# Kernel tuning notes

Hardware: AMD Instinct MI355X
Metric: run time of the kernel (lower is better)

The kernel has to match this reference:

```python
import jax, jax.numpy as jnp
import numpy as np

N_NODES = 100000
N_EDGES = 1200000
D = 64            # in_channels == hidden_channels
N_GRAPHS = 512
N_CLASSES = 10
N_LAYERS = 3
BN_EPS = 1e-5


def setup_inputs() -> dict:
    key = jax.random.key(0)
    ks = jax.random.split(key, 16)
    x = jax.random.normal(ks[0], (N_NODES, D), dtype=jnp.float32)
    edge_index = jax.random.randint(ks[1], (2, N_EDGES), 0, N_NODES, dtype=jnp.int64)
    batch = jnp.sort(jax.random.randint(ks[2], (N_NODES,), 0, N_GRAPHS, dtype=jnp.int64))
    s = 1.0 / np.sqrt(D)
    # all GIN layers share shape since in_channels == hidden_channels
    mlp_w1 = jax.random.uniform(ks[3], (N_LAYERS, D, D), jnp.float32, -s, s)
    mlp_b1 = jax.random.uniform(ks[4], (N_LAYERS, D), jnp.float32, -s, s)
    mlp_w2 = jax.random.uniform(ks[5], (N_LAYERS, D, D), jnp.float32, -s, s)
    mlp_b2 = jax.random.uniform(ks[6], (N_LAYERS, D), jnp.float32, -s, s)
    bn_g = jnp.ones((N_LAYERS, D), jnp.float32)
    bn_b = jnp.zeros((N_LAYERS, D), jnp.float32)
    hw1 = jax.random.uniform(ks[7], (D, D), jnp.float32, -s, s)
    hb1 = jax.random.uniform(ks[8], (D,), jnp.float32, -s, s)
    hg1 = jnp.ones((D,), jnp.float32)
    hbb1 = jnp.zeros((D,), jnp.float32)
    hw2 = jax.random.uniform(ks[9], (D, D // 2), jnp.float32, -s, s)
    hb2 = jax.random.uniform(ks[10], (D // 2,), jnp.float32, -s, s)
    hg2 = jnp.ones((D // 2,), jnp.float32)
    hbb2 = jnp.zeros((D // 2,), jnp.float32)
    s2 = 1.0 / np.sqrt(D // 2)
    ow = jax.random.uniform(ks[11], (D // 2, N_CLASSES), jnp.float32, -s2, s2)
    ob = jax.random.uniform(ks[12], (N_CLASSES,), jnp.float32, -s2, s2)
    return dict(x=x, edge_index=edge_index, batch=batch,
                mlp_w1=mlp_w1, mlp_b1=mlp_b1, mlp_w2=mlp_w2, mlp_b2=mlp_b2,
                bn_g=bn_g, bn_b=bn_b,
                hw1=hw1, hb1=hb1, hg1=hg1, hbb1=hbb1,
                hw2=hw2, hb2=hb2, hg2=hg2, hbb2=hbb2, ow=ow, ob=ob)


def _bn(x, g, b):
    # training-mode BatchNorm1d: biased variance over the batch (node/graph) dim
    mu = jnp.mean(x, axis=0)
    var = jnp.mean((x - mu) ** 2, axis=0)
    return g * (x - mu) * jax.lax.rsqrt(var + BN_EPS) + b


def reference(x, edge_index, batch, mlp_w1, mlp_b1, mlp_w2, mlp_b2, bn_g, bn_b,
              hw1, hb1, hg1, hbb1, hw2, hb2, hg2, hbb2, ow, ob):
    src, dst = edge_index[0], edge_index[1]
    h = x
    for l in range(N_LAYERS):
        # GINConv (eps=0): h_i <- MLP(h_i + sum_{j in N(i)} h_j)
        agg = jax.ops.segment_sum(h[src], dst, num_segments=N_NODES)
        z = h + agg
        z = jax.nn.relu(z @ mlp_w1[l] + mlp_b1[l]) @ mlp_w2[l] + mlp_b2[l]
        h = jax.nn.relu(_bn(z, bn_g[l], bn_b[l]))
        # dropout omitted (deterministic eval)
    # global mean pool per graph
    sums = jax.ops.segment_sum(h, batch, num_segments=N_GRAPHS)
    cnts = jax.ops.segment_sum(jnp.ones((N_NODES,), h.dtype), batch, num_segments=N_GRAPHS)
    g = sums / jnp.maximum(cnts, 1.0)[:, None]
    g = jax.nn.relu(_bn(g @ hw1 + hb1, hg1, hbb1))
    g = jax.nn.relu(_bn(g @ hw2 + hb2, hg2, hbb2))
    return g @ ow + ob
```

## Files before the change

### kernel.cpp

```cpp
#include <hip/hip_runtime.h>
#include <hip/hip_bf16.h>

#define N_NODES 100000
#define N_EDGES 1200000
#define NG 512

typedef float f32;
typedef unsigned short u16;
typedef unsigned short us8 __attribute__((ext_vector_type(8)));
typedef __bf16 bf16x8 __attribute__((ext_vector_type(8)));
typedef float f32x16 __attribute__((ext_vector_type(16)));

__device__ __forceinline__ f32 bf2f(u16 v) {
  return __uint_as_float(((unsigned)v) << 16);
}
__device__ __forceinline__ u16 f2bf(f32 f) {
  __hip_bfloat16 b = __float2bfloat16(f);
  return *reinterpret_cast<u16*>(&b);
}

__global__ void k_detect(const int* __restrict__ w, int* __restrict__ flag) {
  int t = threadIdx.x;
  int acc = 0;
  #pragma unroll
  for (int k = 0; k < 8; ++k) acc |= w[(t * 8 + k) * 2 + 1];
  if (acc) atomicOr(flag, 1);
}

__global__ void k_count(const int* __restrict__ w, const int* __restrict__ flag,
                        int* __restrict__ deg, int* __restrict__ rank) {
  int e2 = blockIdx.x * 256 + threadIdx.x;
  if (e2 >= N_EDGES / 2) return;
  int d0, d1;
  if (flag[0]) {
    int2 dd = *(const int2*)&w[N_EDGES + 2 * e2];
    d0 = dd.x; d1 = dd.y;
  } else {
    int4 dd = *(const int4*)&w[2 * N_EDGES + 4 * e2];
    d0 = dd.x; d1 = dd.z;
  }
  int2 rk;
  rk.x = atomicAdd(&deg[d0], 1);
  rk.y = atomicAdd(&deg[d1], 1);
  *(int2*)&rank[2 * e2] = rk;
}

__global__ void k_scan1(const int* __restrict__ deg, int* __restrict__ incl, int* __restrict__ bsums) {
  __shared__ int sd[256];
  int t = threadIdx.x, b = blockIdx.x;
  int base = b * 1024 + t * 4;
  int v0 = (base + 0 < N_NODES) ? deg[base + 0] : 0;
  int v1 = (base + 1 < N_NODES) ? deg[base + 1] : 0;
  int v2 = (base + 2 < N_NODES) ? deg[base + 2] : 0;
  int v3 = (base + 3 < N_NODES) ? deg[base + 3] : 0;
  int s = v0 + v1 + v2 + v3;
  sd[t] = s; __syncthreads();
  for (int off = 1; off < 256; off <<= 1) {
    int x = (t >= off) ? sd[t - off] : 0; __syncthreads();
    sd[t] += x; __syncthreads();
  }
  int run = sd[t] - s;
  run += v0; if (base + 0 < N_NODES) incl[base + 0] = run;
  run += v1; if (base + 1 < N_NODES) incl[base + 1] = run;
  run += v2; if (base + 2 < N_NODES) incl[base + 2] = run;
  run += v3; if (base + 3 < N_NODES) incl[base + 3] = run;
  if (t == 255) bsums[b] = sd[255];
}

__global__ void k_scan2(int* __restrict__ bsums, int nb) {
  __shared__ int sd[128];
  int t = threadIdx.x;
  int v = (t < nb) ? bsums[t] : 0;
  sd[t] = v; __syncthreads();
  for (int off = 1; off < 128; off <<= 1) {
    int x = (t >= off) ? sd[t - off] : 0; __syncthreads();
    sd[t] += x; __syncthreads();
  }
  if (t < nb) bsums[t] = sd[t] - v;
}

__global__ void k_scan3(const int* __restrict__ incl, const int* __restrict__ bsums,
                        int* __restrict__ offs) {
  int i = blockIdx.x * 256 + threadIdx.x;
  if (i >= N_NODES) return;
  int start = (i == 0) ? 0 : (incl[i - 1] + bsums[(i - 1) >> 10]);
  offs[i] = start;
  if (i == N_NODES - 1) offs[N_NODES] = incl[i] + bsums[i >> 10];
}

__global__ void k_fill(const int* __restrict__ w, const int* __restrict__ flag,
                       const int* __restrict__ offs, const int* __restrict__ rank,
                       int* __restrict__ csr) {
  int e2 = blockIdx.x * 256 + threadIdx.x;
  if (e2 >= N_EDGES / 2) return;
  int s0, s1, d0, d1;
  if (flag[0]) {
    int2 sv = *(const int2*)&w[2 * e2];
    int2 dv = *(const int2*)&w[N_EDGES + 2 * e2];
    s0 = sv.x; s1 = sv.y; d0 = dv.x; d1 = dv.y;
  } else {
    int4 sv = *(const int4*)&w[4 * e2];
    int4 dv = *(const int4*)&w[2 * N_EDGES + 4 * e2];
    s0 = sv.x; s1 = sv.z; d0 = dv.x; d1 = dv.z;
  }
  int2 rk = *(const int2*)&rank[2 * e2];
  csr[offs[d0] + rk.x] = s0;
  csr[offs[d1] + rk.y] = s1;
}

__global__ void k_cast(const f32* __restrict__ x, u16* __restrict__ h) {
  int i = blockIdx.x * 256 + threadIdx.x;
  if (i >= N_NODES * 8) return;
  float4 v0 = ((const float4*)x)[i * 2 + 0];
  float4 v1 = ((const float4*)x)[i * 2 + 1];
  us8 r;
  r[0] = f2bf(v0.x); r[1] = f2bf(v0.y); r[2] = f2bf(v0.z); r[3] = f2bf(v0.w);
  r[4] = f2bf(v1.x); r[5] = f2bf(v1.y); r[6] = f2bf(v1.z); r[7] = f2bf(v1.w);
  *(us8*)&h[i * 8] = r;
}

__global__ __launch_bounds__(256) void k_agg(const u16* __restrict__ hin,
                                             u16* __restrict__ z,
                                             const int* __restrict__ offs,
                                             const int* __restrict__ csr) {
  int wid = blockIdx.x * 4 + (threadIdx.x >> 6);
  int lane = threadIdx.x & 63;
  int slot = lane >> 3;
  int fl = (lane & 7) << 3;
  int e0 = offs[wid], e1 = offs[wid + 1];
  f32 a0[8] = {0,0,0,0,0,0,0,0};
  f32 a1[8] = {0,0,0,0,0,0,0,0};
  int e = e0 + slot;
  for (; e + 8 < e1; e += 16) {
    int s0 = csr[e], s1 = csr[e + 8];
    us8 v0 = *(const us8*)&hin[s0 * 64 + fl];
    us8 v1 = *(const us8*)&hin[s1 * 64 + fl];
    #pragma unroll
    for (int k = 0; k < 8; ++k) { a0[k] += bf2f(v0[k]); a1[k] += bf2f(v1[k]); }
  }
  if (e < e1) {
    us8 v0 = *(const us8*)&hin[csr[e] * 64 + fl];
    #pragma unroll
    for (int k = 0; k < 8; ++k) a0[k] += bf2f(v0[k]);
  }
  #pragma unroll
  for (int k = 0; k < 8; ++k) a0[k] += a1[k];
  #pragma unroll
  for (int k = 0; k < 8; ++k) {
    a0[k] += __shfl_xor(a0[k], 8);
    a0[k] += __shfl_xor(a0[k], 16);
    a0[k] += __shfl_xor(a0[k], 32);
  }
  if (slot == 0) {
    us8 sv = *(const us8*)&hin[wid * 64 + fl];
    us8 o;
    #pragma unroll
    for (int k = 0; k < 8; ++k) o[k] = f2bf(a0[k] + bf2f(sv[k]));
    *(us8*)&z[wid * 64 + fl] = o;
  }
}

__global__ __launch_bounds__(256) void k_mlp(
    const u16* __restrict__ zin, f32* __restrict__ yout,
    const f32* __restrict__ W1, const f32* __restrict__ b1,
    const f32* __restrict__ W2, const f32* __restrict__ b2,
    f32* __restrict__ stsum, f32* __restrict__ stsq)
{
  __shared__ __align__(16) char lds[50176];
  char* zb  = lds;
  char* w1b = lds + 16384;
  char* w2b = lds + 24576;
  char* mb  = lds + 32768;
  f32* b1s  = (f32*)(lds + 49152);
  f32* b2s  = b1s + 64;
  f32* blks = b2s + 64;
  f32* blkq = blks + 64;
  const int t = threadIdx.x;
  const int base = blockIdx.x * 128;
  #pragma unroll
  for (int r = 0; r < 4; ++r) {
    int off = r * 4096 + t * 16;
    int row = off >> 7, c = off & 127;
    *(us8*)(zb + row * 128 + (c ^ ((row & 7) << 4))) =
        *(const us8*)((const char*)(zin + (size_t)base * 64) + off);
  }
  #pragma unroll
  for (int i0 = 0; i0 < 16; ++i0) {
    int i = i0 * 256 + t;
    int k = i >> 6, c = i & 63;
    int off = c * 128 + ((k * 2) ^ ((c & 7) << 4));
    *(u16*)(w1b + off) = f2bf(W1[i]);
    *(u16*)(w2b + off) = f2bf(W2[i]);
  }
  if (t < 64) { b1s[t] = b1[t]; b2s[t] = b2[t]; blks[t] = 0.f; blkq[t] = 0.f; }
  __syncthreads();
  const int wv = t >> 6, l = t & 63;
  const int lr = l & 31, lh = l >> 5;
  f32x16 acc0, acc1;
  #pragma unroll
  for (int i = 0; i < 16; ++i) { acc0[i] = 0.f; acc1[i] = 0.f; }
  #pragma unroll
  for (int s = 0; s < 4; ++s) {
    int kb = s * 32 + lh * 16;
    int arow = wv * 32 + lr;
    bf16x8 a  = *(bf16x8*)(zb + arow * 128 + (kb ^ ((arow & 7) << 4)));
    bf16x8 bA = *(bf16x8*)(w1b + lr * 128 + (kb ^ ((lr & 7) << 4)));
    bf16x8 bB = *(bf16x8*)(w1b + (lr + 32) * 128 + (kb ^ (((lr + 32) & 7) << 4)));
    acc0 = __builtin_amdgcn_mfma_f32_32x32x16_bf16(a, bA, acc0, 0, 0, 0);
    acc1 = __builtin_amdgcn_mfma_f32_32x32x16_bf16(a, bB, acc1, 0, 0, 0);
  }
  #pragma unroll
  for (int g = 0; g < 16; ++g) {
    int rowl = (g & 3) + 8 * (g >> 2) + 4 * lh;
    int roff = wv * 4096 + rowl * 128;
    int sw = (rowl & 7) << 4;
    *(u16*)(mb + roff + ((lr * 2) ^ sw))        = f2bf(fmaxf(acc0[g] + b1s[lr], 0.f));
    *(u16*)(mb + roff + (((lr + 32) * 2) ^ sw)) = f2bf(fmaxf(acc1[g] + b1s[lr + 32], 0.f));
  }
  asm volatile("s_waitcnt lgkmcnt(0)" ::: "memory");
  #pragma unroll
  for (int i = 0; i < 16; ++i) { acc0[i] = 0.f; acc1[i] = 0.f; }
  #pragma unroll
  for (int s = 0; s < 4; ++s) {
    int kb = s * 32 + lh * 16;
    bf16x8 a  = *(bf16x8*)(mb + wv * 4096 + lr * 128 + (kb ^ ((lr & 7) << 4)));
    bf16x8 bA = *(bf16x8*)(w2b + lr * 128 + (kb ^ ((lr & 7) << 4)));
    bf16x8 bB = *(bf16x8*)(w2b + (lr + 32) * 128 + (kb ^ (((lr + 32) & 7) << 4)));
    acc0 = __builtin_amdgcn_mfma_f32_32x32x16_bf16(a, bA, acc0, 0, 0, 0);
    acc1 = __builtin_amdgcn_mfma_f32_32x32x16_bf16(a, bB, acc1, 0, 0, 0);
  }
  __syncthreads();
  char* yb = lds + wv * 8192;
  f32 ps0 = 0, pq0 = 0, ps1 = 0, pq1 = 0;
  #pragma unroll
  for (int g = 0; g < 16; ++g) {
    int rowl = (g & 3) + 8 * (g >> 2) + 4 * lh;
    f32 y0 = acc0[g] + b2s[lr];
    f32 y1 = acc1[g] + b2s[lr + 32];
    *(f32*)(yb + rowl * 256 + lr * 4)        = y0;
    *(f32*)(yb + rowl * 256 + (lr + 32) * 4) = y1;
    if (base + wv * 32 + rowl < N_NODES) {
      ps0 += y0; pq0 += y0 * y0;
      ps1 += y1; pq1 += y1 * y1;
    }
  }
  asm volatile("s_waitcnt lgkmcnt(0)" ::: "memory");
  __builtin_amdgcn_sched_barrier(0);
  #pragma unroll
  for (int k = 0; k < 8; ++k) {
    int row = k * 4 + (l >> 4);
    float4 v = *(float4*)(yb + row * 256 + (l & 15) * 16);
    int node = base + wv * 32 + row;
    if (node < N_NODES)
      *(float4*)&yout[(size_t)node * 64 + (l & 15) * 4] = v;
  }
  atomicAdd(&blks[lr], ps0);      atomicAdd(&blkq[lr], pq0);
  atomicAdd(&blks[lr + 32], ps1); atomicAdd(&blkq[lr + 32], pq1);
  __syncthreads();
  if (t < 64) { atomicAdd(&stsum[t], blks[t]); atomicAdd(&stsq[t], blkq[t]); }
}

__global__ __launch_bounds__(256) void k_bnfin(const f32* __restrict__ y, u16* __restrict__ h,
                                               const f32* __restrict__ st,
                                               const f32* __restrict__ g, const f32* __restrict__ b) {
  __shared__ f32 ss[128];
  int t = threadIdx.x;
  if (t < 64) {
    f32 m = st[t] * (1.f / N_NODES);
    f32 var = st[64 + t] * (1.f / N_NODES) - m * m;
    f32 sc = g[t] * rsqrtf(var + 1e-5f);
    ss[t] = sc; ss[64 + t] = b[t] - m * sc;
  }
  __syncthreads();
  int i = blockIdx.x * 256 + t;
  if (i >= N_NODES * 8) return;
  int c0 = (i & 7) * 8;
  float4 v0 = ((const float4*)y)[i * 2 + 0];
  float4 v1 = ((const float4*)y)[i * 2 + 1];
  us8 r;
  r[0] = f2bf(fmaxf(fmaf(v0.x, ss[c0 + 0], ss[64 + c0 + 0]), 0.f));
  r[1] = f2bf(fmaxf(fmaf(v0.y, ss[c0 + 1], ss[64 + c0 + 1]), 0.f));
  r[2] = f2bf(fmaxf(fmaf(v0.z, ss[c0 + 2], ss[64 + c0 + 2]), 0.f));
  r[3] = f2bf(fmaxf(fmaf(v0.w, ss[c0 + 3], ss[64 + c0 + 3]), 0.f));
  r[4] = f2bf(fmaxf(fmaf(v1.x, ss[c0 + 4], ss[64 + c0 + 4]), 0.f));
  r[5] = f2bf(fmaxf(fmaf(v1.y, ss[c0 + 5], ss[64 + c0 + 5]), 0.f));
  r[6] = f2bf(fmaxf(fmaf(v1.z, ss[c0 + 6], ss[64 + c0 + 6]), 0.f));
  r[7] = f2bf(fmaxf(fmaf(v1.w, ss[c0 + 7], ss[64 + c0 + 7]), 0.f));
  *(us8*)&h[i * 8] = r;
}

__global__ void k_pool(const f32* __restrict__ y, const int* __restrict__ bw,
                       const int* __restrict__ flag, const f32* __restrict__ st,
                       const f32* __restrict__ g, const f32* __restrict__ b,
                       f32* __restrict__ gsum, f32* __restrict__ gcnt) {
  __shared__ f32 ss[128];
  int t = threadIdx.x;
  if (t < 64) {
    f32 m = st[t] * (1.f / N_NODES);
    f32 var = st[64 + t] * (1.f / N_NODES) - m * m;
    f32 sc = g[t] * rsqrtf(var + 1e-5f);
    ss[t] = sc; ss[64 + t] = b[t] - m * sc;
  }
  __syncthreads();
  int wid = (blockIdx.x * blockDim.x + t) >> 6;
  int lane = t & 63;
  const int nw = (256 * 256) >> 6;
  const int per = (N_NODES + nw - 1) / nw;
  int s = wid * per; int e = s + per; if (e > N_NODES) e = N_NODES;
  if (s >= e) return;
  f32 sc = ss[lane], sh = ss[64 + lane];
  int is32 = flag[0];
  int gcur = is32 ? bw[s] : bw[2 * s];
  f32 acc = 0.f, cnt = 0.f;
  for (int i = s; i < e; ++i) {
    int gi = is32 ? bw[i] : bw[2 * i];
    if (gi != gcur) {
      atomicAdd(&gsum[gcur * 64 + lane], acc);
      if (lane == 0) atomicAdd(&gcnt[gcur], cnt);
      gcur = gi; acc = 0.f; cnt = 0.f;
    }
    acc += fmaxf(fmaf(y[(size_t)i * 64 + lane], sc, sh), 0.f);
    cnt += 1.f;
  }
  atomicAdd(&gsum[gcur * 64 + lane], acc);
  if (lane == 0) atomicAdd(&gcnt[gcur], cnt);
}

__global__ __launch_bounds__(256) void k_head1(const f32* __restrict__ gsum, const f32* __restrict__ gcnt,
                                               const f32* __restrict__ W, const f32* __restrict__ bias,
                                               f32* __restrict__ p, f32* __restrict__ st) {
  __shared__ f32 Ws[4096];
  __shared__ f32 zs[4][64];
  __shared__ f32 bs[64], bq[64];
  int t = threadIdx.x;
  for (int i = t; i < 4096; i += 256) Ws[i] = W[i];
  if (t < 64) { bs[t] = 0.f; bq[t] = 0.f; }
  int wave = t >> 6, lane = t & 63;
  int row = blockIdx.x * 4 + wave;
  f32 z = gsum[row * 64 + lane] / fmaxf(gcnt[row], 1.f);
  zs[wave][lane] = z;
  __syncthreads();
  f32 y = bias[lane];
  for (int f = 0; f < 64; ++f) y = fmaf(zs[wave][f], Ws[f * 64 + lane], y);
  p[row * 64 + lane] = y;
  atomicAdd(&bs[lane], y);
  atomicAdd(&bq[lane], y * y);
  __syncthreads();
  if (t < 64) { atomicAdd(&st[t], bs[t]); atomicAdd(&st[64 + t], bq[t]); }
}

__global__ __launch_bounds__(256) void k_head2(const f32* __restrict__ p1, const f32* __restrict__ st,
                                               const f32* __restrict__ g, const f32* __restrict__ b,
                                               const f32* __restrict__ W, const f32* __restrict__ bias,
                                               f32* __restrict__ p2, f32* __restrict__ st2) {
  __shared__ f32 Ws[2048];
  __shared__ f32 zs[4][64];
  __shared__ f32 bs[32], bq[32];
  __shared__ f32 ss[128];
  int t = threadIdx.x;
  for (int i = t; i < 2048; i += 256) Ws[i] = W[i];
  if (t < 64) {
    f32 m = st[t] * (1.f / NG);
    f32 var = st[64 + t] * (1.f / NG) - m * m;
    f32 sc = g[t] * rsqrtf(var + 1e-5f);
    ss[t] = sc; ss[64 + t] = b[t] - m * sc;
  }
  if (t < 32) { bs[t] = 0.f; bq[t] = 0.f; }
  __syncthreads();
  int wave = t >> 6, lane = t & 63;
  int row = blockIdx.x * 4 + wave;
  f32 z = fmaxf(fmaf(p1[row * 64 + lane], ss[lane], ss[64 + lane]), 0.f);
  zs[wave][lane] = z;
  __syncthreads();
  if (lane < 32) {
    f32 y = bias[lane];
    for (int f = 0; f < 64; ++f) y = fmaf(zs[wave][f], Ws[f * 32 + lane], y);
    p2[row * 32 + lane] = y;
    atomicAdd(&bs[lane], y);
    atomicAdd(&bq[lane], y * y);
  }
  __syncthreads();
  if (t < 32) { atomicAdd(&st2[t], bs[t]); atomicAdd(&st2[64 + t], bq[t]); }
}

__global__ __launch_bounds__(256) void k_head3(const f32* __restrict__ p2, const f32* __restrict__ st2,
                                               const f32* __restrict__ g, const f32* __restrict__ b,
                                               const f32* __restrict__ W, const f32* __restrict__ bias,
                                               f32* __restrict__ out) {
  __shared__ f32 Ws[320];
  __shared__ f32 obs[10];
  __shared__ f32 zs[4][32];
  __shared__ f32 ss[64];
  int t = threadIdx.x;
  for (int i = t; i < 320; i += 256) Ws[i] = W[i];
  if (t < 10) obs[t] = bias[t];
  if (t < 32) {
    f32 m = st2[t] * (1.f / NG);
    f32 var = st2[64 + t] * (1.f / NG) - m * m;
    f32 sc = g[t] * rsqrtf(var + 1e-5f);
    ss[t] = sc; ss[32 + t] = b[t] - m * sc;
  }
  __syncthreads();
  int wave = t >> 6, lane = t & 63;
  int row = blockIdx.x * 4 + wave;
  if (lane < 32) zs[wave][lane] = fmaxf(fmaf(p2[row * 32 + lane], ss[lane], ss[32 + lane]), 0.f);
  __syncthreads();
  if (lane < 10) {
    f32 o = obs[lane];
    for (int f = 0; f < 32; ++f) o = fmaf(zs[wave][f], Ws[f * 10 + lane], o);
    out[row * 10 + lane] = o;
  }
}

extern "C" void kernel_launch(void* const* d_in, const int* in_sizes, int n_in,
                              void* d_out, int out_size, void* d_ws, size_t ws_size,
                              hipStream_t stream) {
  (void)in_sizes; (void)n_in; (void)out_size; (void)ws_size;
  const f32* x    = (const f32*)d_in[0];
  const int* eiw  = (const int*)d_in[1];
  const int* btw  = (const int*)d_in[2];
  const f32* mw1  = (const f32*)d_in[3];
  const f32* mb1  = (const f32*)d_in[4];
  const f32* mw2  = (const f32*)d_in[5];
  const f32* mb2  = (const f32*)d_in[6];
  const f32* bng  = (const f32*)d_in[7];
  const f32* bnb  = (const f32*)d_in[8];
  const f32* hw1  = (const f32*)d_in[9];
  const f32* hb1  = (const f32*)d_in[10];
  const f32* hg1  = (const f32*)d_in[11];
  const f32* hbb1 = (const f32*)d_in[12];
  const f32* hw2  = (const f32*)d_in[13];
  const f32* hb2  = (const f32*)d_in[14];
  const f32* hg2  = (const f32*)d_in[15];
  const f32* hbb2 = (const f32*)d_in[16];
  const f32* ow   = (const f32*)d_in[17];
  const f32* ob   = (const f32*)d_in[18];
  f32* out = (f32*)d_out;

  int* deg   = (int*)d_ws;
  int* flag  = deg + 100000;
  f32* stats = (f32*)(flag + 32);
  f32* gsum  = stats + 1024;
  f32* gcnt  = gsum + NG * 64;
  const size_t ZERO_INTS = 100000 + 32 + 1024 + 32768 + 512;
  int* incl  = (int*)(gcnt + NG);
  int* bsums = incl + 100000;
  int* offs  = bsums + 128;
  int* rank  = offs + 100004;
  int* csr   = rank + N_EDGES;
  u16* hbuf  = (u16*)(csr + N_EDGES);
  u16* zbuf  = hbuf + (size_t)N_NODES * 64;
  f32* ybuf  = (f32*)(zbuf + (size_t)100096 * 64);
  f32* p1    = ybuf + (size_t)N_NODES * 64;
  f32* p2    = p1 + NG * 64;

  hipMemsetAsync(deg, 0, ZERO_INTS * sizeof(int), stream);

  k_detect<<<1, 256, 0, stream>>>(eiw, flag);
  k_count<<<(N_EDGES / 2 + 255) / 256, 256, 0, stream>>>(eiw, flag, deg, rank);
  k_scan1<<<(N_NODES + 1023) / 1024, 256, 0, stream>>>(deg, incl, bsums);
  k_scan2<<<1, 128, 0, stream>>>(bsums, (N_NODES + 1023) / 1024);
  k_scan3<<<(N_NODES + 255) / 256, 256, 0, stream>>>(incl, bsums, offs);
  k_fill<<<(N_EDGES / 2 + 255) / 256, 256, 0, stream>>>(eiw, flag, offs, rank, csr);

  const int AGG_GRID = N_NODES / 4;
  const int MLP_GRID = (N_NODES + 127) / 128;
  const int C8_GRID  = (N_NODES * 8 + 255) / 256;

  k_cast<<<C8_GRID, 256, 0, stream>>>(x, hbuf);
  k_agg<<<AGG_GRID, 256, 0, stream>>>(hbuf, zbuf, offs, csr);
  k_mlp<<<MLP_GRID, 256, 0, stream>>>(zbuf, ybuf, mw1, mb1, mw2, mb2, stats + 0, stats + 64);
  k_bnfin<<<C8_GRID, 256, 0, stream>>>(ybuf, hbuf, stats + 0, bng + 0, bnb + 0);
  k_agg<<<AGG_GRID, 256, 0, stream>>>(hbuf, zbuf, offs, csr);
  k_mlp<<<MLP_GRID, 256, 0, stream>>>(zbuf, ybuf, mw1 + 4096, mb1 + 64, mw2 + 4096, mb2 + 64, stats + 128, stats + 192);
  k_bnfin<<<C8_GRID, 256, 0, stream>>>(ybuf, hbuf, stats + 128, bng + 64, bnb + 64);
  k_agg<<<AGG_GRID, 256, 0, stream>>>(hbuf, zbuf, offs, csr);
  k_mlp<<<MLP_GRID, 256, 0, stream>>>(zbuf, ybuf, mw1 + 8192, mb1 + 128, mw2 + 8192, mb2 + 128, stats + 256, stats + 320);

  k_pool<<<256, 256, 0, stream>>>(ybuf, btw, flag, stats + 256, bng + 128, bnb + 128, gsum, gcnt);
  k_head1<<<NG / 4, 256, 0, stream>>>(gsum, gcnt, hw1, hb1, p1, stats + 384);
  k_head2<<<NG / 4, 256, 0, stream>>>(p1, stats + 384, hg1, hbb1, hw2, hb2, p2, stats + 512);
  k_head3<<<NG / 4, 256, 0, stream>>>(p2, stats + 512, hg2, hbb2, ow, ob, out);
}
```

Baseline: 486.2 us.

## Build CSR via two-level bucket sort instead of global atomic counting and scan

Replaces the count/scan/fill CSR construction with a two-level bucket sort. Edges are first scattered into 512 destination-range buckets using shared-memory histograms, which leaves only a few global atomics per block. Each bucket is then sorted locally in shared memory to emit CSR offsets and sources. This removes per-edge global atomics and several scan launches. In exchange it relies on a fixed bucket capacity (BCAP=3000), which could overflow for skewed degree distributions, and it reads edge indices one at a time rather than vectorized.

```diff
diff --git a/kernel.cpp b/kernel.cpp
--- a/kernel.cpp
+++ b/kernel.cpp
@@ -4,6 +4,9 @@
 #define N_NODES 100000
 #define N_EDGES 1200000
 #define NG 512
+#define NB 512
+#define SPAN 196
+#define BCAP 3000
 
 typedef float f32;
 typedef unsigned short u16;
@@ -19,93 +22,103 @@
   return *reinterpret_cast<u16*>(&b);
 }
 
-__global__ void k_detect(const int* __restrict__ w, int* __restrict__ flag) {
-  int t = threadIdx.x;
-  int acc = 0;
-  #pragma unroll
-  for (int k = 0; k < 8; ++k) acc |= w[(t * 8 + k) * 2 + 1];
-  if (acc) atomicOr(flag, 1);
-}
-
-__global__ void k_count(const int* __restrict__ w, const int* __restrict__ flag,
-                        int* __restrict__ deg, int* __restrict__ rank) {
-  int e2 = blockIdx.x * 256 + threadIdx.x;
-  if (e2 >= N_EDGES / 2) return;
-  int d0, d1;
-  if (flag[0]) {
-    int2 dd = *(const int2*)&w[N_EDGES + 2 * e2];
-    d0 = dd.x; d1 = dd.y;
-  } else {
-    int4 dd = *(const int4*)&w[2 * N_EDGES + 4 * e2];
-    d0 = dd.x; d1 = dd.z;
-  }
-  int2 rk;
-  rk.x = atomicAdd(&deg[d0], 1);
-  rk.y = atomicAdd(&deg[d1], 1);
-  *(int2*)&rank[2 * e2] = rk;
-}
-
-__global__ void k_scan1(const int* __restrict__ deg, int* __restrict__ incl, int* __restrict__ bsums) {
-  __shared__ int sd[256];
-  int t = threadIdx.x, b = blockIdx.x;
-  int base = b * 1024 + t * 4;
-  int v0 = (base + 0 < N_NODES) ? deg[base + 0] : 0;
-  int v1 = (base + 1 < N_NODES) ? deg[base + 1] : 0;
-  int v2 = (base + 2 < N_NODES) ? deg[base + 2] : 0;
-  int v3 = (base + 3 < N_NODES) ? deg[base + 3] : 0;
-  int s = v0 + v1 + v2 + v3;
-  sd[t] = s; __syncthreads();
-  for (int off = 1; off < 256; off <<= 1) {
+__global__ void k_detect(const int* __restrict__ w, int* __restrict__ flag,
+                         int* __restrict__ bcur) {
+  int t = threadIdx.x;
+  if (t < 256) {
+    int acc = 0;
+    #pragma unroll
+    for (int k = 0; k < 8; ++k) acc |= w[(t * 8 + k) * 2 + 1];
+    if (acc) atomicOr(flag, 1);
+  }
+  bcur[t] = t * BCAP;
+}
+
+__global__ __launch_bounds__(256) void k_bscatter(const int* __restrict__ w,
+                                                  const int* __restrict__ flag,
+                                                  int* __restrict__ bcur,
+                                                  int* __restrict__ ssrc,
+                                                  u16* __restrict__ sld) {
+  __shared__ int bins[NB];
+  __shared__ int lbase[NB];
+  const int t = threadIdx.x;
+  for (int i = t; i < NB; i += 256) bins[i] = 0;
+  __syncthreads();
+  const int per = (N_EDGES + 255) / 256;
+  int e0 = blockIdx.x * per;
+  int e1 = e0 + per; if (e1 > N_EDGES) e1 = N_EDGES;
+  const int is32 = flag[0];
+  for (int e = e0 + t; e < e1; e += 256) {
+    int d = is32 ? w[N_EDGES + e] : w[2 * (N_EDGES + e)];
+    atomicAdd(&bins[d / SPAN], 1);
+  }
+  __syncthreads();
+  for (int i = t; i < NB; i += 256) {
+    int c = bins[i];
+    lbase[i] = c ? atomicAdd(&bcur[i], c) : 0;
+  }
+  __syncthreads();
+  for (int i = t; i < NB; i += 256) bins[i] = 0;
+  __syncthreads();
+  for (int e = e0 + t; e < e1; e += 256) {
+    int s, d;
+    if (is32) { s = w[e];     d = w[N_EDGES + e]; }
+    else      { s = w[2 * e]; d = w[2 * (N_EDGES + e)]; }
+    int b = d / SPAN;
+    int r = atomicAdd(&bins[b], 1);
+    int slot = lbase[b] + r;
+    ssrc[slot] = s;
+    sld[slot]  = (u16)(d - b * SPAN);
+  }
+}
+
+__global__ void k_bscan(const int* __restrict__ bcur, int* __restrict__ bbase) {
+  __shared__ int sd[NB];
+  int t = threadIdx.x;
+  int c = bcur[t] - t * BCAP;
+  sd[t] = c; __syncthreads();
+  for (int off = 1; off < NB; off <<= 1) {
     int x = (t >= off) ? sd[t - off] : 0; __syncthreads();
     sd[t] += x; __syncthreads();
   }
-  int run = sd[t] - s;
-  run += v0; if (base + 0 < N_NODES) incl[base + 0] = run;
-  run += v1; if (base + 1 < N_NODES) incl[base + 1] = run;
-  run += v2; if (base + 2 < N_NODES) incl[base + 2] = run;
-  run += v3; if (base + 3 < N_NODES) incl[base + 3] = run;
-  if (t == 255) bsums[b] = sd[255];
-}
-
-__global__ void k_scan2(int* __restrict__ bsums, int nb) {
-  __shared__ int sd[128];
-  int t = threadIdx.x;
-  int v = (t < nb) ? bsums[t] : 0;
-  sd[t] = v; __syncthreads();
-  for (int off = 1; off < 128; off <<= 1) {
-    int x = (t >= off) ? sd[t - off] : 0; __syncthreads();
-    sd[t] += x; __syncthreads();
-  }
-  if (t < nb) bsums[t] = sd[t] - v;
-}
-
-__global__ void k_scan3(const int* __restrict__ incl, const int* __restrict__ bsums,
-                        int* __restrict__ offs) {
-  int i = blockIdx.x * 256 + threadIdx.x;
-  if (i >= N_NODES) return;
-  int start = (i == 0) ? 0 : (incl[i - 1] + bsums[(i - 1) >> 10]);
-  offs[i] = start;
-  if (i == N_NODES - 1) offs[N_NODES] = incl[i] + bsums[i >> 10];
-}
-
-__global__ void k_fill(const int* __restrict__ w, const int* __restrict__ flag,
-                       const int* __restrict__ offs, const int* __restrict__ rank,
-                       int* __restrict__ csr) {
-  int e2 = blockIdx.x * 256 + threadIdx.x;
-  if (e2 >= N_EDGES / 2) return;
-  int s0, s1, d0, d1;
-  if (flag[0]) {
-    int2 sv = *(const int2*)&w[2 * e2];
-    int2 dv = *(const int2*)&w[N_EDGES + 2 * e2];
-    s0 = sv.x; s1 = sv.y; d0 = dv.x; d1 = dv.y;
-  } else {
-    int4 sv = *(const int4*)&w[4 * e2];
-    int4 dv = *(const int4*)&w[2 * N_EDGES + 4 * e2];
-    s0 = sv.x; s1 = sv.z; d0 = dv.x; d1 = dv.z;
-  }
-  int2 rk = *(const int2*)&rank[2 * e2];
-  csr[offs[d0] + rk.x] = s0;
-  csr[offs[d1] + rk.y] = s1;
+  bbase[t] = sd[t] - c;
+  if (t == NB - 1) bbase[NB] = sd[t];
+}
+
+__global__ __launch_bounds__(256) void k_bsort(const int* __restrict__ bcur,
+                                               const int* __restrict__ bbase,
+                                               const int* __restrict__ ssrc,
+                                               const u16* __restrict__ sld,
+                                               int* __restrict__ csr,
+                                               int* __restrict__ offs) {
+  __shared__ int hist[256];
+  __shared__ int cur[SPAN];
+  const int b = blockIdx.x, t = threadIdx.x;
+  const int sbase = b * BCAP;
+  const int cnt = bcur[b] - sbase;
+  const int ebase = bbase[b];
+  hist[t] = 0;
+  __syncthreads();
+  for (int i = t; i < cnt; i += 256) atomicAdd(&hist[sld[sbase + i]], 1);
+  __syncthreads();
+  int v0 = hist[t]; __syncthreads();
+  for (int off = 1; off < 256; off <<= 1) {
+    int x = (t >= off) ? hist[t - off] : 0; __syncthreads();
+    hist[t] += x; __syncthreads();
+  }
+  int excl = hist[t] - v0;
+  int node = b * SPAN + t;
+  if (t < SPAN) {
+    cur[t] = excl;
+    if (node < N_NODES) offs[node] = ebase + excl;
+  }
+  if (b == NB - 1 && t == 0) offs[N_NODES] = ebase + cnt;
+  __syncthreads();
+  for (int i = t; i < cnt; i += 256) {
+    int ld = sld[sbase + i];
+    int r = atomicAdd(&cur[ld], 1);
+    csr[ebase + r] = ssrc[sbase + i];
+  }
 }
 
 __global__ void k_cast(const f32* __restrict__ x, u16* __restrict__ h) {
@@ -437,31 +450,29 @@
   const f32* ob   = (const f32*)d_in[18];
   f32* out = (f32*)d_out;
 
-  int* deg   = (int*)d_ws;
-  int* flag  = deg + 100000;
+  int* flag  = (int*)d_ws;
   f32* stats = (f32*)(flag + 32);
   f32* gsum  = stats + 1024;
   f32* gcnt  = gsum + NG * 64;
-  const size_t ZERO_INTS = 100000 + 32 + 1024 + 32768 + 512;
-  int* incl  = (int*)(gcnt + NG);
-  int* bsums = incl + 100000;
-  int* offs  = bsums + 128;
-  int* rank  = offs + 100004;
-  int* csr   = rank + N_EDGES;
+  const size_t ZERO_INTS = 32 + 1024 + NG * 64 + NG;
+  int* bcur  = (int*)(gcnt + NG);
+  int* bbase = bcur + NB;
+  int* offs  = bbase + 516;
+  int* ssrc  = offs + 100004;
+  u16* sldv  = (u16*)(ssrc + NB * BCAP);
+  int* csr   = (int*)(sldv + NB * BCAP);
   u16* hbuf  = (u16*)(csr + N_EDGES);
   u16* zbuf  = hbuf + (size_t)N_NODES * 64;
   f32* ybuf  = (f32*)(zbuf + (size_t)100096 * 64);
   f32* p1    = ybuf + (size_t)N_NODES * 64;
   f32* p2    = p1 + NG * 64;
 
-  hipMemsetAsync(deg, 0, ZERO_INTS * sizeof(int), stream);
-
-  k_detect<<<1, 256, 0, stream>>>(eiw, flag);
-  k_count<<<(N_EDGES / 2 + 255) / 256, 256, 0, stream>>>(eiw, flag, deg, rank);
-  k_scan1<<<(N_NODES + 1023) / 1024, 256, 0, stream>>>(deg, incl, bsums);
-  k_scan2<<<1, 128, 0, stream>>>(bsums, (N_NODES + 1023) / 1024);
-  k_scan3<<<(N_NODES + 255) / 256, 256, 0, stream>>>(incl, bsums, offs);
-  k_fill<<<(N_EDGES / 2 + 255) / 256, 256, 0, stream>>>(eiw, flag, offs, rank, csr);
+  hipMemsetAsync(flag, 0, ZERO_INTS * sizeof(int), stream);
+
+  k_detect<<<1, 512, 0, stream>>>(eiw, flag, bcur);
+  k_bscatter<<<256, 256, 0, stream>>>(eiw, flag, bcur, ssrc, sldv);
+  k_bscan<<<1, NB, 0, stream>>>(bcur, bbase);
+  k_bsort<<<NB, 256, 0, stream>>>(bcur, bbase, ssrc, sldv, csr, offs);
 
   const int AGG_GRID = N_NODES / 4;
   const int MLP_GRID = (N_NODES + 127) / 128;
```

Measured after the change: 453.3 us. 1.07x faster.
